# Kernel tuning notes

Hardware: AMD Instinct MI355X
Metric: run time of the kernel (lower is better)

## Reference

```python
import jax, jax.numpy as jnp
import numpy as np

N, V, E_PER = 8, 4608, 73728          # batch, nodes per graph, edges per graph
D_IN, C, NCLS = 1, 512, 3             # node feat dim, embed dim, classes
E = N * E_PER
LN_EPS = 1e-5


def setup_inputs() -> dict:
    key = jax.random.key(0)
    ks = jax.random.split(key, 12)
    x = jax.random.normal(ks[0], (N, 1, V, D_IN), jnp.float32)
    edge_index = jax.random.randint(ks[1], (2, E), 0, V, dtype=jnp.int32)
    edge_weight = jax.random.uniform(ks[2], (E,), jnp.float32)
    # GCNConv params: layer0 maps D_IN->C, layers 1..2 map C->C (weight [in,out], bias [out])
    w0 = jax.random.normal(ks[3], (D_IN, C), jnp.float32) * 0.02
    b0 = jnp.zeros((C,), jnp.float32)
    w1 = jax.random.normal(ks[4], (C, C), jnp.float32) * 0.02
    b1 = jnp.zeros((C,), jnp.float32)
    w2 = jax.random.normal(ks[5], (C, C), jnp.float32) * 0.02
    b2 = jnp.zeros((C,), jnp.float32)
    ln_g = jnp.ones((C,), jnp.float32)
    ln_b = jnp.zeros((C,), jnp.float32)
    head_w = jax.random.normal(ks[6], (C, NCLS), jnp.float32) * 2e-5
    head_b = jnp.log(jnp.full((NCLS,), 1.0 / NCLS, jnp.float32))
    return {"x": x, "edge_weight": edge_weight, "w0": w0, "b0": b0,
            "w1": w1, "b1": b1, "w2": w2, "b2": b2,
            "ln_g": ln_g, "ln_b": ln_b, "head_w": head_w, "head_b": head_b,
            "edge_index": edge_index}


def layer_norm(h, g, b):
    mu = h.mean(-1, keepdims=True)
    var = ((h - mu) ** 2).mean(-1, keepdims=True)
    return (h - mu) * jax.lax.rsqrt(var + LN_EPS) * g + b


def reference(x, edge_weight, w0, b0, w1, b1, w2, b2, ln_g, ln_b, head_w, head_b, edge_index):
    n, t, v, d = x.shape
    nv = n * v
    h = x.reshape(nv, d)
    # batch-offset local edge indices (edges are contiguous per graph)
    offs = jnp.repeat(jnp.arange(n, dtype=edge_index.dtype) * v, edge_index.shape[1] // n)
    src = edge_index[0] + offs
    tgt = edge_index[1] + offs
    # GCN norm with self-loops (fill weight 1.0), symmetric deg^-1/2 normalization
    loop = jnp.arange(nv, dtype=src.dtype)
    src_f = jnp.concatenate([src, loop])
    tgt_f = jnp.concatenate([tgt, loop])
    ew_f = jnp.concatenate([edge_weight, jnp.ones((nv,), edge_weight.dtype)])
    deg = jax.ops.segment_sum(ew_f, tgt_f, num_segments=nv)
    deg_safe = jnp.where(deg > 0, deg, 1.0)
    dinv = jnp.where(deg > 0, jax.lax.rsqrt(deg_safe), 0.0)
    norm = dinv[src_f] * ew_f * dinv[tgt_f]
    for w, bb in ((w0, b0), (w1, b1), (w2, b2)):
        hw = h @ w                                   # [NV, C]
        msg = norm[:, None] * hw[src_f]              # gather + scale  [E+NV, C]
        h = jax.ops.segment_sum(msg, tgt_f, num_segments=nv) + bb
        h = jax.nn.relu(h)
        h = layer_norm(h, ln_g, ln_b)
        # dropout is identity in eval mode
    pooled = h.reshape(n, v, -1).max(axis=1)         # global_max_pool (contiguous batch)
    pooled = layer_norm(pooled, ln_g, ln_b)
    return pooled @ head_w + head_b                  # [N, NCLS]
```

## Files before the change

### kernel.cpp

```cpp
#include <hip/hip_runtime.h>
#include <hip/hip_bf16.h>
#include <stdint.h>

#define N_GRAPH 8
#define V_NODES 4608
#define E_PER   73728
#define NV      (N_GRAPH * V_NODES)
#define E_TOT   (N_GRAPH * E_PER)
#define C       512
#define NCLS    3
#define LN_EPS  1e-5f
#define POOL_CHUNKS 36
#define SCAN_BLOCKS 144

typedef __attribute__((ext_vector_type(8))) short short8;
typedef __attribute__((ext_vector_type(4))) float floatx4;
typedef __attribute__((address_space(1))) void v_g;
typedef __attribute__((address_space(3))) void v_l;


__device__ inline float waveReduceSum(float v) {
#pragma unroll
    for (int o = 32; o > 0; o >>= 1) v += __shfl_down(v, o, 64);
    return v;
}

__device__ inline float blockSum512(float v, volatile float* sred) {
    float s = waveReduceSum(v);
    if ((threadIdx.x & 63) == 0) sred[threadIdx.x >> 6] = s;
    __syncthreads();
    float t = 0.f;
#pragma unroll
    for (int i = 0; i < 8; i++) t += sred[i];
    __syncthreads();
    return t;
}

__device__ inline unsigned short f2bf(float f) {
    uint32_t u = __float_as_uint(f);
    u += 0x7fffu + ((u >> 16) & 1u);
    return (unsigned short)(u >> 16);
}
__device__ inline float bf2f(unsigned short b) {
    return __uint_as_float(((uint32_t)b) << 16);
}


__global__ void k_init(float* dinv, int* counts) {
    int i = blockIdx.x * 256 + threadIdx.x;
    if (i < NV) { dinv[i] = 1.0f; counts[i] = 0; }
}

__global__ void k_deg_count(const int* __restrict__ ei, const float* __restrict__ ew,
                            float* __restrict__ dinv, int* __restrict__ counts) {
    int e = blockIdx.x * 256 + threadIdx.x;
    if (e >= E_TOT) return;
    int off = (e / E_PER) * V_NODES;
    int t = ei[E_TOT + e] + off;
    atomicAdd(&dinv[t], ew[e]);
    atomicAdd(&counts[t], 1);
}

__global__ void k_rsqrt(float* dinv) {
    int i = blockIdx.x * 256 + threadIdx.x;
    if (i < NV) dinv[i] = rsqrtf(dinv[i]);
}


__global__ void k_scan1(const int* __restrict__ counts, int* __restrict__ row_ptr,
                        int* __restrict__ bsum) {
    __shared__ int sh[256];
    const int b = blockIdx.x, tid = threadIdx.x;
    const int idx = b * 256 + tid;
    int v = counts[idx];
    sh[tid] = v;
    __syncthreads();
#pragma unroll
    for (int off = 1; off < 256; off <<= 1) {
        int t = (tid >= off) ? sh[tid - off] : 0;
        __syncthreads();
        sh[tid] += t;
        __syncthreads();
    }
    row_ptr[idx] = sh[tid] - v;
    if (tid == 255) bsum[b] = sh[255];
}

__global__ void k_scan2(int* __restrict__ bsum) {
    __shared__ int sh[256];
    const int tid = threadIdx.x;
    int v = (tid < SCAN_BLOCKS) ? bsum[tid] : 0;
    sh[tid] = v;
    __syncthreads();
#pragma unroll
    for (int off = 1; off < 256; off <<= 1) {
        int t = (tid >= off) ? sh[tid - off] : 0;
        __syncthreads();
        sh[tid] += t;
        __syncthreads();
    }
    if (tid < SCAN_BLOCKS) bsum[tid] = sh[tid] - v;
}

__global__ void k_scan3(int* __restrict__ row_ptr, const int* __restrict__ bsum,
                        int* __restrict__ cursor) {
    const int b = blockIdx.x, tid = threadIdx.x;
    const int idx = b * 256 + tid;
    int v = row_ptr[idx] + bsum[b];
    row_ptr[idx] = v;
    cursor[idx] = v;
    if (idx == 0) row_ptr[NV] = E_TOT;
}

__global__ void k_fill(const int* __restrict__ ei, const float* __restrict__ ew,
                       const float* __restrict__ dinv, int* __restrict__ cursor,
                       int* __restrict__ col_idx, float* __restrict__ val) {
    int e = blockIdx.x * 256 + threadIdx.x;
    if (e >= E_TOT) return;
    int off = (e / E_PER) * V_NODES;
    int s = ei[e] + off;
    int t = ei[E_TOT + e] + off;
    int pos = atomicAdd(&cursor[t], 1);
    col_idx[pos] = s;
    val[pos] = dinv[s] * ew[e] * dinv[t];
}


__global__ void k_wt(const float* __restrict__ w1, const float* __restrict__ w2,
                     unsigned short* __restrict__ wt1, unsigned short* __restrict__ wt2) {
    int idx = blockIdx.x * 256 + threadIdx.x;
    int which = idx >> 18;
    int rem = idx & 0x3ffff;
    int n = rem >> 9, k = rem & 511;
    const float* W = which ? w2 : w1;
    unsigned short* WT = which ? wt2 : wt1;
    WT[n * C + k] = f2bf(W[k * C + n]);
}


__global__ void k_agg0_scalar(const float* __restrict__ x, const int* __restrict__ row_ptr,
                              const int* __restrict__ col_idx, const float* __restrict__ val,
                              const float* __restrict__ dinv, float* __restrict__ s0) {
    int t = blockIdx.x * 256 + threadIdx.x;
    if (t >= NV) return;
    float dt = dinv[t];
    float acc = dt * dt * x[t];
    int e1 = row_ptr[t + 1];
    for (int e = row_ptr[t]; e < e1; e++)
        acc += val[e] * x[col_idx[e]];
    s0[t] = acc;
}

__launch_bounds__(128)
__global__ void k_l0post(const float* __restrict__ s0, const float* __restrict__ w0,
                         const float* __restrict__ b0, const float* __restrict__ ln_g,
                         const float* __restrict__ ln_b, unsigned short* __restrict__ out) {
    const int t = blockIdx.x;
    const int tid = threadIdx.x;
    const int c4 = tid << 2;
    float s = s0[t];
    float4 w = *reinterpret_cast<const float4*>(&w0[c4]);
    float4 bb = *reinterpret_cast<const float4*>(&b0[c4]);
    float vx = fmaxf(s * w.x + bb.x, 0.f);
    float vy = fmaxf(s * w.y + bb.y, 0.f);
    float vz = fmaxf(s * w.z + bb.z, 0.f);
    float vw = fmaxf(s * w.w + bb.w, 0.f);
    __shared__ float redA[2], redB[2];
    float wsum = waveReduceSum(vx + vy + vz + vw);
    if ((tid & 63) == 0) redA[tid >> 6] = wsum;
    __syncthreads();
    float mu = (redA[0] + redA[1]) * (1.0f / C);
    float dx = vx - mu, dy = vy - mu, dz = vz - mu, dw = vw - mu;
    float wsq = waveReduceSum(dx * dx + dy * dy + dz * dz + dw * dw);
    if ((tid & 63) == 0) redB[tid >> 6] = wsq;
    __syncthreads();
    float rstd = rsqrtf((redB[0] + redB[1]) * (1.0f / C) + LN_EPS);
    float4 g = *reinterpret_cast<const float4*>(&ln_g[c4]);
    float4 b = *reinterpret_cast<const float4*>(&ln_b[c4]);
    ushort4 o = { f2bf(dx * rstd * g.x + b.x), f2bf(dy * rstd * g.y + b.y),
                  f2bf(dz * rstd * g.z + b.z), f2bf(dw * rstd * g.w + b.w) };
    reinterpret_cast<ushort4*>(out)[(size_t)t * 128 + tid] = o;
}


__launch_bounds__(256)
__global__ void k_gemm_mfma(const unsigned short* __restrict__ A,
                            const unsigned short* __restrict__ WT,
                            unsigned short* __restrict__ Bout) {
    __shared__ short8 lA[512];
    __shared__ short8 lB[512];
    const int tid = threadIdx.x;
    const int lane = tid & 63;
    const int wave = tid >> 6;
    const int wr = wave >> 1, wc = wave & 1;
    const int l15 = lane & 15, kg = lane >> 4;
    const int m0 = blockIdx.x * 128;
    const int n0 = blockIdx.y * 128;

    floatx4 acc[4][4] = {};

    const int s0i = tid, s1i = 256 + tid;
    const int kgs0 = s0i >> 7, idx0 = s0i & 127;
    const int kgs1 = s1i >> 7, idx1 = s1i & 127;
    const unsigned short* gA0 = A + (size_t)(m0 + idx0) * C + kgs0 * 8;
    const unsigned short* gA1 = A + (size_t)(m0 + idx1) * C + kgs1 * 8;
    const unsigned short* gB0 = WT + (size_t)(n0 + idx0) * C + kgs0 * 8;
    const unsigned short* gB1 = WT + (size_t)(n0 + idx1) * C + kgs1 * 8;

    for (int k0 = 0; k0 < C; k0 += 32) {
        __builtin_amdgcn_global_load_lds((v_g*)(gA0 + k0), (v_l*)&lA[s0i], 16, 0, 0);
        __builtin_amdgcn_global_load_lds((v_g*)(gA1 + k0), (v_l*)&lA[s1i], 16, 0, 0);
        __builtin_amdgcn_global_load_lds((v_g*)(gB0 + k0), (v_l*)&lB[s0i], 16, 0, 0);
        __builtin_amdgcn_global_load_lds((v_g*)(gB1 + k0), (v_l*)&lB[s1i], 16, 0, 0);
        asm volatile("s_waitcnt vmcnt(0)" ::: "memory");
        __syncthreads();

        short8 af[4], bf[4];
#pragma unroll
        for (int mi = 0; mi < 4; mi++)
            af[mi] = lA[kg * 128 + wr * 64 + mi * 16 + l15];
#pragma unroll
        for (int ni = 0; ni < 4; ni++)
            bf[ni] = lB[kg * 128 + wc * 64 + ni * 16 + l15];
#pragma unroll
        for (int mi = 0; mi < 4; mi++)
#pragma unroll
            for (int ni = 0; ni < 4; ni++)
                acc[mi][ni] = __builtin_amdgcn_mfma_f32_16x16x32_bf16(
                    af[mi], bf[ni], acc[mi][ni], 0, 0, 0);
        __syncthreads();
    }

#pragma unroll
    for (int mi = 0; mi < 4; mi++) {
#pragma unroll
        for (int ni = 0; ni < 4; ni++) {
            int n = n0 + wc * 64 + ni * 16 + l15;
#pragma unroll
            for (int r = 0; r < 4; r++) {
                int m = m0 + wr * 64 + mi * 16 + kg * 4 + r;
                Bout[(size_t)m * C + n] = f2bf(acc[mi][ni][r]);
            }
        }
    }
}


__launch_bounds__(128)
__global__ void k_agg(const unsigned short* __restrict__ hw, const int* __restrict__ row_ptr,
                      const int* __restrict__ col_idx, const float* __restrict__ val,
                      const float* __restrict__ dinv, const float* __restrict__ bias,
                      const float* __restrict__ ln_g, const float* __restrict__ ln_b,
                      unsigned short* __restrict__ out) {
    const int b = blockIdx.x;
    const int t = (b & 7) * V_NODES + (b >> 3);
    const int tid = threadIdx.x;
    const int e0 = row_ptr[t], e1 = row_ptr[t + 1];
    const ushort4* hw4 = reinterpret_cast<const ushort4*>(hw);
    const float dt = dinv[t];
    const float selfw = dt * dt;
    ushort4 hs = hw4[(size_t)t * 128 + tid];
    float ax = selfw * bf2f(hs.x), ay = selfw * bf2f(hs.y);
    float az = selfw * bf2f(hs.z), aw = selfw * bf2f(hs.w);

    __shared__ int   sh_s[128];
    __shared__ float sh_v[128];
    for (int base = e0; base < e1; base += 128) {
        int cnt = min(128, e1 - base);
        if (tid < cnt) { sh_s[tid] = col_idx[base + tid]; sh_v[tid] = val[base + tid]; }
        __syncthreads();
        int j = 0;
        for (; j + 2 <= cnt; j += 2) {
            float w0 = sh_v[j], w1 = sh_v[j + 1];
            ushort4 h0 = hw4[(size_t)sh_s[j] * 128 + tid];
            ushort4 h1 = hw4[(size_t)sh_s[j + 1] * 128 + tid];
            ax += w0 * bf2f(h0.x); ay += w0 * bf2f(h0.y);
            az += w0 * bf2f(h0.z); aw += w0 * bf2f(h0.w);
            ax += w1 * bf2f(h1.x); ay += w1 * bf2f(h1.y);
            az += w1 * bf2f(h1.z); aw += w1 * bf2f(h1.w);
        }
        if (j < cnt) {
            float w = sh_v[j];
            ushort4 hv = hw4[(size_t)sh_s[j] * 128 + tid];
            ax += w * bf2f(hv.x); ay += w * bf2f(hv.y);
            az += w * bf2f(hv.z); aw += w * bf2f(hv.w);
        }
        __syncthreads();
    }
    int c4 = tid << 2;
    float4 bb = *reinterpret_cast<const float4*>(&bias[c4]);
    ax = fmaxf(ax + bb.x, 0.f); ay = fmaxf(ay + bb.y, 0.f);
    az = fmaxf(az + bb.z, 0.f); aw = fmaxf(aw + bb.w, 0.f);
    __shared__ float redA[2], redB[2];
    float wsum = waveReduceSum(ax + ay + az + aw);
    if ((tid & 63) == 0) redA[tid >> 6] = wsum;
    __syncthreads();
    float mu = (redA[0] + redA[1]) * (1.0f / C);
    float dx = ax - mu, dy = ay - mu, dz = az - mu, dw = aw - mu;
    float wsq = waveReduceSum(dx * dx + dy * dy + dz * dz + dw * dw);
    if ((tid & 63) == 0) redB[tid >> 6] = wsq;
    __syncthreads();
    float rstd = rsqrtf((redB[0] + redB[1]) * (1.0f / C) + LN_EPS);
    float4 g = *reinterpret_cast<const float4*>(&ln_g[c4]);
    float4 b2 = *reinterpret_cast<const float4*>(&ln_b[c4]);
    ushort4 o = { f2bf(dx * rstd * g.x + b2.x), f2bf(dy * rstd * g.y + b2.y),
                  f2bf(dz * rstd * g.z + b2.z), f2bf(dw * rstd * g.w + b2.w) };
    reinterpret_cast<ushort4*>(out)[(size_t)t * 128 + tid] = o;
}


__global__ void k_pool1(const unsigned short* __restrict__ h, float* __restrict__ pmax) {
    int g = blockIdx.x, chunk = blockIdx.y;
    int c = threadIdx.x;
    int r0 = g * V_NODES + chunk * 128;
    float m = -1e30f;
#pragma unroll 4
    for (int r = 0; r < 128; r++)
        m = fmaxf(m, bf2f(h[(size_t)(r0 + r) * C + c]));
    pmax[((size_t)g * POOL_CHUNKS + chunk) * C + c] = m;
}

__global__ void k_pool2_head(const float* __restrict__ pmax, const float* __restrict__ ln_g,
                             const float* __restrict__ ln_b, const float* __restrict__ hw,
                             const float* __restrict__ hb, float* __restrict__ out) {
    __shared__ float sred[8];
    int g = blockIdx.x;
    int c = threadIdx.x;
    float m = -1e30f;
#pragma unroll
    for (int j = 0; j < POOL_CHUNKS; j++)
        m = fmaxf(m, pmax[((size_t)g * POOL_CHUNKS + j) * C + c]);
    float total = blockSum512(m, sred);
    float mu = total * (1.0f / C);
    float d = m - mu;
    float var = blockSum512(d * d, sred) * (1.0f / C);
    float rstd = rsqrtf(var + LN_EPS);
    float p = d * rstd * ln_g[c] + ln_b[c];
    float r0 = blockSum512(p * hw[c * NCLS + 0], sred);
    float r1 = blockSum512(p * hw[c * NCLS + 1], sred);
    float r2 = blockSum512(p * hw[c * NCLS + 2], sred);
    if (threadIdx.x == 0) {
        out[g * NCLS + 0] = r0 + hb[0];
        out[g * NCLS + 1] = r1 + hb[1];
        out[g * NCLS + 2] = r2 + hb[2];
    }
}


extern "C" void kernel_launch(void* const* d_in, const int* in_sizes, int n_in,
                              void* d_out, int out_size, void* d_ws, size_t ws_size,
                              hipStream_t stream) {
    const float* x      = (const float*)d_in[0];
    const float* ew     = (const float*)d_in[1];
    const float* w0     = (const float*)d_in[2];
    const float* b0     = (const float*)d_in[3];
    const float* w1     = (const float*)d_in[4];
    const float* b1     = (const float*)d_in[5];
    const float* w2     = (const float*)d_in[6];
    const float* b2     = (const float*)d_in[7];
    const float* ln_g   = (const float*)d_in[8];
    const float* ln_b   = (const float*)d_in[9];
    const float* head_w = (const float*)d_in[10];
    const float* head_b = (const float*)d_in[11];
    const int*   ei     = (const int*)d_in[12];
    float* out = (float*)d_out;

    char* p = (char*)d_ws;
    auto alloc = [&](size_t bytes) { void* r = p; p += (bytes + 255) & ~255ull; return r; };
    unsigned short* bufA = (unsigned short*)alloc((size_t)NV * C * 2);
    unsigned short* bufB = (unsigned short*)alloc((size_t)NV * C * 2);
    unsigned short* wt1  = (unsigned short*)alloc((size_t)C * C * 2);
    unsigned short* wt2  = (unsigned short*)alloc((size_t)C * C * 2);
    float* s0      = (float*)alloc((size_t)NV * 4);
    float* dinv    = (float*)alloc((size_t)NV * 4);
    int*   counts  = (int*)alloc((size_t)NV * 4);
    int*   row_ptr = (int*)alloc((size_t)(NV + 1) * 4);
    int*   cursor  = (int*)alloc((size_t)NV * 4);
    int*   bsum    = (int*)alloc((size_t)SCAN_BLOCKS * 4);
    int*   col_idx = (int*)alloc((size_t)E_TOT * 4);
    float* val     = (float*)alloc((size_t)E_TOT * 4);
    float* pmax    = (float*)alloc((size_t)N_GRAPH * POOL_CHUNKS * C * 4);

    k_init<<<NV / 256, 256, 0, stream>>>(dinv, counts);
    k_deg_count<<<E_TOT / 256, 256, 0, stream>>>(ei, ew, dinv, counts);
    k_rsqrt<<<NV / 256, 256, 0, stream>>>(dinv);
    k_scan1<<<SCAN_BLOCKS, 256, 0, stream>>>(counts, row_ptr, bsum);
    k_scan2<<<1, 256, 0, stream>>>(bsum);
    k_scan3<<<SCAN_BLOCKS, 256, 0, stream>>>(row_ptr, bsum, cursor);
    k_fill<<<E_TOT / 256, 256, 0, stream>>>(ei, ew, dinv, cursor, col_idx, val);
    k_wt<<<(2 * C * C) / 256, 256, 0, stream>>>(w1, w2, wt1, wt2);

    k_agg0_scalar<<<NV / 256, 256, 0, stream>>>(x, row_ptr, col_idx, val, dinv, s0);
    k_l0post<<<NV, 128, 0, stream>>>(s0, w0, b0, ln_g, ln_b, bufA);

    k_gemm_mfma<<<dim3(NV / 128, C / 128), 256, 0, stream>>>(bufA, wt1, bufB);
    k_agg<<<NV, 128, 0, stream>>>(bufB, row_ptr, col_idx, val, dinv, b1, ln_g, ln_b, bufA);

    k_gemm_mfma<<<dim3(NV / 128, C / 128), 256, 0, stream>>>(bufA, wt2, bufB);
    k_agg<<<NV, 128, 0, stream>>>(bufB, row_ptr, col_idx, val, dinv, b2, ln_g, ln_b, bufA);

    k_pool1<<<dim3(N_GRAPH, POOL_CHUNKS), C, 0, stream>>>(bufA, pmax);
    k_pool2_head<<<N_GRAPH, C, 0, stream>>>(pmax, ln_g, ln_b, head_w, head_b, out);
}
```

Baseline: 458.8 us.

## Aggregate one node per wavefront with 16-byte loads and shuffle-only layernorm

```diff
diff --git a/kernel.cpp b/kernel.cpp
--- a/kernel.cpp
+++ b/kernel.cpp
@@ -22,6 +22,12 @@
 __device__ inline float waveReduceSum(float v) {
 #pragma unroll
     for (int o = 32; o > 0; o >>= 1) v += __shfl_down(v, o, 64);
+    return v;
+}
+
+__device__ inline float waveAllSum(float v) {
+#pragma unroll
+    for (int o = 32; o > 0; o >>= 1) v += __shfl_xor(v, o, 64);
     return v;
 }
 
@@ -246,66 +252,80 @@
 }
 
 
-__launch_bounds__(128)
+__launch_bounds__(256)
 __global__ void k_agg(const unsigned short* __restrict__ hw, const int* __restrict__ row_ptr,
                       const int* __restrict__ col_idx, const float* __restrict__ val,
                       const float* __restrict__ dinv, const float* __restrict__ bias,
                       const float* __restrict__ ln_g, const float* __restrict__ ln_b,
                       unsigned short* __restrict__ out) {
     const int b = blockIdx.x;
-    const int t = (b & 7) * V_NODES + (b >> 3);
-    const int tid = threadIdx.x;
+    const int wv = threadIdx.x >> 6;
+    const int lane = threadIdx.x & 63;
+    const int t = (b & 7) * V_NODES + ((b >> 3) << 2) + wv;
     const int e0 = row_ptr[t], e1 = row_ptr[t + 1];
-    const ushort4* hw4 = reinterpret_cast<const ushort4*>(hw);
+    const short8* hw8 = reinterpret_cast<const short8*>(hw);
+
     const float dt = dinv[t];
     const float selfw = dt * dt;
-    ushort4 hs = hw4[(size_t)t * 128 + tid];
-    float ax = selfw * bf2f(hs.x), ay = selfw * bf2f(hs.y);
-    float az = selfw * bf2f(hs.z), aw = selfw * bf2f(hs.w);
-
-    __shared__ int   sh_s[128];
-    __shared__ float sh_v[128];
-    for (int base = e0; base < e1; base += 128) {
-        int cnt = min(128, e1 - base);
-        if (tid < cnt) { sh_s[tid] = col_idx[base + tid]; sh_v[tid] = val[base + tid]; }
-        __syncthreads();
-        int j = 0;
-        for (; j + 2 <= cnt; j += 2) {
-            float w0 = sh_v[j], w1 = sh_v[j + 1];
-            ushort4 h0 = hw4[(size_t)sh_s[j] * 128 + tid];
-            ushort4 h1 = hw4[(size_t)sh_s[j + 1] * 128 + tid];
-            ax += w0 * bf2f(h0.x); ay += w0 * bf2f(h0.y);
-            az += w0 * bf2f(h0.z); aw += w0 * bf2f(h0.w);
-            ax += w1 * bf2f(h1.x); ay += w1 * bf2f(h1.y);
-            az += w1 * bf2f(h1.z); aw += w1 * bf2f(h1.w);
-        }
-        if (j < cnt) {
-            float w = sh_v[j];
-            ushort4 hv = hw4[(size_t)sh_s[j] * 128 + tid];
-            ax += w * bf2f(hv.x); ay += w * bf2f(hv.y);
-            az += w * bf2f(hv.z); aw += w * bf2f(hv.w);
-        }
-        __syncthreads();
-    }
-    int c4 = tid << 2;
-    float4 bb = *reinterpret_cast<const float4*>(&bias[c4]);
-    ax = fmaxf(ax + bb.x, 0.f); ay = fmaxf(ay + bb.y, 0.f);
-    az = fmaxf(az + bb.z, 0.f); aw = fmaxf(aw + bb.w, 0.f);
-    __shared__ float redA[2], redB[2];
-    float wsum = waveReduceSum(ax + ay + az + aw);
-    if ((tid & 63) == 0) redA[tid >> 6] = wsum;
-    __syncthreads();
-    float mu = (redA[0] + redA[1]) * (1.0f / C);
-    float dx = ax - mu, dy = ay - mu, dz = az - mu, dw = aw - mu;
-    float wsq = waveReduceSum(dx * dx + dy * dy + dz * dz + dw * dw);
-    if ((tid & 63) == 0) redB[tid >> 6] = wsq;
-    __syncthreads();
-    float rstd = rsqrtf((redB[0] + redB[1]) * (1.0f / C) + LN_EPS);
-    float4 g = *reinterpret_cast<const float4*>(&ln_g[c4]);
-    float4 b2 = *reinterpret_cast<const float4*>(&ln_b[c4]);
-    ushort4 o = { f2bf(dx * rstd * g.x + b2.x), f2bf(dy * rstd * g.y + b2.y),
-                  f2bf(dz * rstd * g.z + b2.z), f2bf(dw * rstd * g.w + b2.w) };
-    reinterpret_cast<ushort4*>(out)[(size_t)t * 128 + tid] = o;
+    short8 hs = hw8[(size_t)t * 64 + lane];
+    float a[8];
+#pragma unroll
+    for (int i = 0; i < 8; i++) a[i] = selfw * bf2f((unsigned short)hs[i]);
+
+    int e = e0;
+    for (; e + 4 <= e1; e += 4) {
+        int i0 = col_idx[e], i1 = col_idx[e + 1], i2 = col_idx[e + 2], i3 = col_idx[e + 3];
+        float w0 = val[e], w1 = val[e + 1], w2 = val[e + 2], w3 = val[e + 3];
+        short8 h0 = hw8[(size_t)i0 * 64 + lane];
+        short8 h1 = hw8[(size_t)i1 * 64 + lane];
+        short8 h2 = hw8[(size_t)i2 * 64 + lane];
+        short8 h3 = hw8[(size_t)i3 * 64 + lane];
+#pragma unroll
+        for (int i = 0; i < 8; i++) a[i] += w0 * bf2f((unsigned short)h0[i]);
+#pragma unroll
+        for (int i = 0; i < 8; i++) a[i] += w1 * bf2f((unsigned short)h1[i]);
+#pragma unroll
+        for (int i = 0; i < 8; i++) a[i] += w2 * bf2f((unsigned short)h2[i]);
+#pragma unroll
+        for (int i = 0; i < 8; i++) a[i] += w3 * bf2f((unsigned short)h3[i]);
+    }
+    for (; e < e1; e++) {
+        int is = col_idx[e];
+        float w = val[e];
+        short8 hv = hw8[(size_t)is * 64 + lane];
+#pragma unroll
+        for (int i = 0; i < 8; i++) a[i] += w * bf2f((unsigned short)hv[i]);
+    }
+
+    const int c8 = lane << 3;
+    float4 bb0 = *reinterpret_cast<const float4*>(&bias[c8]);
+    float4 bb1 = *reinterpret_cast<const float4*>(&bias[c8 + 4]);
+    a[0] = fmaxf(a[0] + bb0.x, 0.f); a[1] = fmaxf(a[1] + bb0.y, 0.f);
+    a[2] = fmaxf(a[2] + bb0.z, 0.f); a[3] = fmaxf(a[3] + bb0.w, 0.f);
+    a[4] = fmaxf(a[4] + bb1.x, 0.f); a[5] = fmaxf(a[5] + bb1.y, 0.f);
+    a[6] = fmaxf(a[6] + bb1.z, 0.f); a[7] = fmaxf(a[7] + bb1.w, 0.f);
+
+    float s = a[0] + a[1] + a[2] + a[3] + a[4] + a[5] + a[6] + a[7];
+    float mu = waveAllSum(s) * (1.0f / C);
+    float sq = 0.f;
+#pragma unroll
+    for (int i = 0; i < 8; i++) { float d = a[i] - mu; sq += d * d; }
+    float rstd = rsqrtf(waveAllSum(sq) * (1.0f / C) + LN_EPS);
+
+    float4 g0 = *reinterpret_cast<const float4*>(&ln_g[c8]);
+    float4 g1 = *reinterpret_cast<const float4*>(&ln_g[c8 + 4]);
+    float4 z0 = *reinterpret_cast<const float4*>(&ln_b[c8]);
+    float4 z1 = *reinterpret_cast<const float4*>(&ln_b[c8 + 4]);
+    short8 o;
+    o[0] = (short)f2bf((a[0] - mu) * rstd * g0.x + z0.x);
+    o[1] = (short)f2bf((a[1] - mu) * rstd * g0.y + z0.y);
+    o[2] = (short)f2bf((a[2] - mu) * rstd * g0.z + z0.z);
+    o[3] = (short)f2bf((a[3] - mu) * rstd * g0.w + z0.w);
+    o[4] = (short)f2bf((a[4] - mu) * rstd * g1.x + z1.x);
+    o[5] = (short)f2bf((a[5] - mu) * rstd * g1.y + z1.y);
+    o[6] = (short)f2bf((a[6] - mu) * rstd * g1.z + z1.z);
+    o[7] = (short)f2bf((a[7] - mu) * rstd * g1.w + z1.w);
+    reinterpret_cast<short8*>(out)[(size_t)t * 64 + lane] = o;
 }
 
 
@@ -394,10 +414,10 @@
     k_l0post<<<NV, 128, 0, stream>>>(s0, w0, b0, ln_g, ln_b, bufA);
 
     k_gemm_mfma<<<dim3(NV / 128, C / 128), 256, 0, stream>>>(bufA, wt1, bufB);
-    k_agg<<<NV, 128, 0, stream>>>(bufB, row_ptr, col_idx, val, dinv, b1, ln_g, ln_b, bufA);
+    k_agg<<<NV / 4, 256, 0, stream>>>(bufB, row_ptr, col_idx, val, dinv, b1, ln_g, ln_b, bufA);
 
     k_gemm_mfma<<<dim3(NV / 128, C / 128), 256, 0, stream>>>(bufA, wt2, bufB);
-    k_agg<<<NV, 128, 0, stream>>>(bufB, row_ptr, col_idx, val, dinv, b2, ln_g, ln_b, bufA);
+    k_agg<<<NV / 4, 256, 0, stream>>>(bufB, row_ptr, col_idx, val, dinv, b2, ln_g, ln_b, bufA);
 
     k_pool1<<<dim3(N_GRAPH, POOL_CHUNKS), C, 0, stream>>>(bufA, pmax);
     k_pool2_head<<<N_GRAPH, C, 0, stream>>>(pmax, ln_g, ln_b, head_w, head_b, out);
```

Measured after the change: 432.5 us. 5.7% less time.
